# Kernel tuning notes

Measured on AMD Instinct MI355X. Metric: run time of the kernel, lower is better.

Reference implementation:

```python
import jax, jax.numpy as jnp
import numpy as np

EPS = 1e-6
D = 512      # embedding_dim
M = 4        # n_modules
B = 4        # batch
S = 128      # seq_len
K = 32       # stack_size
STEPS = 16   # max_steps (ACT)
SCALE = D ** (-0.5)


def _clin(zr, zi, Wr, Wi, sub):
    # complex linear: (Wr + i Wi)(zr + i zi), torch Linear convention y = x @ W.T
    yr = jnp.einsum(sub, zr, Wr) - jnp.einsum(sub, zi, Wi)
    yi = jnp.einsum(sub, zi, Wr) + jnp.einsum(sub, zr, Wi)
    return yr, yi


def forward_fn(x_real, x_imag, Wl_r, Wl_i, Wq_r, Wq_i, Wk_r, Wk_i, Wv_r, Wv_i,
               ln_scale, ln_shift, mod_bias, gate_mask,
               score_w, score_b, conf_w, conf_b, halt_w, halt_b,
               ctrl_w, ctrl_b, st_score_w, st_score_b, st_conf_w, st_conf_b):
    mem0 = jnp.zeros((B, K, 2 * D), x_real.dtype)
    ptr0 = jnp.zeros((B, K), x_real.dtype).at[:, 0].set(1.0)
    acc0 = jnp.zeros((B, S, 2 * D), x_real.dtype)
    rem0 = jnp.ones((B,), x_real.dtype)

    def step(carry, _):
        sr, si, mem, ptr, acc, rem = carry
        # ComplexAttentionBlock (all M modules vectorized on axis m)
        cr = 0.5 * x_real + 0.5 * sr
        ci = 0.5 * x_imag + 0.5 * si
        zr, zi = _clin(cr, ci, Wl_r, Wl_i, 'bsd,mod->bmso')   # [B,M,S,D]
        # ComplexLayerNorm (magnitude LN, unbiased var as torch.var default)
        mag = jnp.sqrt(zr * zr + zi * zi) + EPS
        mean = mag.mean(-1, keepdims=True)
        var = mag.var(-1, keepdims=True, ddof=1)
        nm = (mag - mean) / jnp.sqrt(var + EPS)
        nm = nm * ln_scale[None, :, None, :] + ln_shift[None, :, None, :]
        ph = jnp.arctan2(zi, zr)
        zr = nm * jnp.cos(ph)
        zi = nm * jnp.sin(ph)
        # ModReLU
        nrm = jnp.sqrt(zr * zr + zi * zi) + EPS
        sc = jax.nn.relu(nrm + mod_bias[None, :, None, :]) / nrm
        zr = zr * sc
        zi = zi * sc
        # ComplexAttention over concatenated real/imag q,k
        sub = 'bmsd,mod->bmso'
        qr, qi = _clin(zr, zi, Wq_r, Wq_i, sub)
        kr, ki = _clin(zr, zi, Wk_r, Wk_i, sub)
        vr, vi = _clin(zr, zi, Wv_r, Wv_i, sub)
        qf = jnp.concatenate([qr, qi], -1)   # [B,M,S,2D]
        kf = jnp.concatenate([kr, ki], -1)
        attn = jax.nn.softmax(jnp.einsum('bmse,bmte->bmst', qf, kf) * SCALE, axis=-1)
        ar = jnp.einsum('bmst,bmtd->bmsd', attn, vr)
        ai = jnp.einsum('bmst,bmtd->bmsd', attn, vi)
        # SigmoidGatingMask
        g = jax.nn.sigmoid(gate_mask)[None, :, None, :]
        pr = ar * g
        pi = ai * g
        flat = jnp.concatenate([pr, pi], -1)  # [B,M,S,2D]
        score = jnp.einsum('bmse,me->bms', flat, score_w) + score_b[None, :, None]
        conf = jax.nn.sigmoid(jnp.einsum('bmse,me->bms', flat, conf_w) + conf_b[None, :, None])
        halt = jnp.einsum('bmse,me->bms', flat, halt_w) + halt_b[None, :, None]
        # DifferentiableStack on seq-pooled broadcast state
        flat_in = jnp.concatenate([sr.mean(1), si.mean(1)], -1)  # [B,2D]
        control = jax.nn.softmax(flat_in @ ctrl_w + ctrl_b, axis=-1)  # [B,3]
        push, pop, noop = control[:, 0:1], control[:, 1:2], control[:, 2:3]
        ptr_up = jnp.roll(ptr, 1, axis=1)
        ptr_dn = jnp.roll(ptr, -1, axis=1)
        new_ptr = push * ptr_up + pop * ptr_dn + noop * ptr
        new_ptr = new_ptr / (new_ptr.sum(1, keepdims=True) + EPS)
        wmask = push * ptr_up                                   # [B,K]
        new_mem = wmask[..., None] * flat_in[:, None, :] + mem * (1.0 - wmask[..., None])
        read = (new_mem * new_ptr[..., None]).sum(1)            # [B,2D]
        sp_r, sp_i = read[:, :D], read[:, D:]
        st_sc = read @ st_score_w + st_score_b[0]               # [B]
        st_cf = jax.nn.sigmoid(read @ st_conf_w + st_conf_b[0])
        # combine M block proposals + stack proposal via score*confidence softmax
        all_pr = jnp.concatenate([pr, jnp.broadcast_to(sp_r[:, None, None, :], (B, 1, S, D))], 1)
        all_pi = jnp.concatenate([pi, jnp.broadcast_to(sp_i[:, None, None, :], (B, 1, S, D))], 1)
        all_sc = jnp.concatenate([score, jnp.broadcast_to(st_sc[:, None, None], (B, 1, S))], 1)
        all_cf = jnp.concatenate([conf, jnp.broadcast_to(st_cf[:, None, None], (B, 1, S))], 1)
        w = jax.nn.softmax(all_sc * all_cf, axis=1)[..., None]  # [B,M+1,S,1]
        new_sr = (w * all_pr).sum(1)
        new_si = (w * all_pi).sum(1)
        # ACT halting accumulation
        p = jax.nn.sigmoid(halt).mean(axis=(1, 2))              # [B]
        acc = acc + (p * rem)[:, None, None] * jnp.concatenate([new_sr, new_si], -1)
        rem = rem * (1.0 - p)
        return (new_sr, new_si, new_mem, new_ptr, acc, rem), None

    carry, _ = jax.lax.scan(step, (x_real, x_imag, mem0, ptr0, acc0, rem0), None, length=STEPS)
    sr, si, _, _, acc, rem = carry
    # add ACT remainder weight on final state
    out = acc + rem[:, None, None] * jnp.concatenate([sr, si], -1)
    return out  # [B,S,2D] real/imag concat


def setup_inputs() -> dict:
    key = jax.random.key(0)
    ks = jax.random.split(key, 24)
    w = 1.0 / np.sqrt(D)
    h = 0.02
    inp = {
        'x_real': jax.random.normal(ks[0], (B, S, D), jnp.float32),
        'x_imag': jax.random.normal(ks[1], (B, S, D), jnp.float32),
        'Wl_r': jax.random.normal(ks[2], (M, D, D), jnp.float32) * w,
        'Wl_i': jax.random.normal(ks[3], (M, D, D), jnp.float32) * w,
        'Wq_r': jax.random.normal(ks[4], (M, D, D), jnp.float32) * w,
        'Wq_i': jax.random.normal(ks[5], (M, D, D), jnp.float32) * w,
        'Wk_r': jax.random.normal(ks[6], (M, D, D), jnp.float32) * w,
        'Wk_i': jax.random.normal(ks[7], (M, D, D), jnp.float32) * w,
        'Wv_r': jax.random.normal(ks[8], (M, D, D), jnp.float32) * w,
        'Wv_i': jax.random.normal(ks[9], (M, D, D), jnp.float32) * w,
        'ln_scale': jnp.ones((M, D), jnp.float32),
        'ln_shift': jnp.zeros((M, D), jnp.float32),
        'mod_bias': jnp.zeros((M, D), jnp.float32),
        'gate_mask': jnp.ones((M, D), jnp.float32),
        'score_w': jax.random.normal(ks[10], (M, 2 * D), jnp.float32) * h,
        'score_b': jnp.zeros((M,), jnp.float32),
        'conf_w': jax.random.normal(ks[11], (M, 2 * D), jnp.float32) * h,
        'conf_b': jnp.zeros((M,), jnp.float32),
        'halt_w': jax.random.normal(ks[12], (M, 2 * D), jnp.float32) * h,
        'halt_b': jnp.full((M,), -4.0, jnp.float32),  # nn.init.constant_(halt_head.bias, -4.0)
        'ctrl_w': jax.random.normal(ks[13], (2 * D, 3), jnp.float32) * h,
        'ctrl_b': jnp.zeros((3,), jnp.float32),
        'st_score_w': jax.random.normal(ks[14], (2 * D,), jnp.float32) * h,
        'st_score_b': jnp.zeros((1,), jnp.float32),
        'st_conf_w': jax.random.normal(ks[15], (2 * D,), jnp.float32) * h,
        'st_conf_b': jnp.zeros((1,), jnp.float32),
    }
    return inp


def reference(x_real, x_imag, Wl_r, Wl_i, Wq_r, Wq_i, Wk_r, Wk_i, Wv_r, Wv_i,
              ln_scale, ln_shift, mod_bias, gate_mask,
              score_w, score_b, conf_w, conf_b, halt_w, halt_b,
              ctrl_w, ctrl_b, st_score_w, st_score_b, st_conf_w, st_conf_b):
    return forward_fn(x_real, x_imag, Wl_r, Wl_i, Wq_r, Wq_i, Wk_r, Wk_i, Wv_r, Wv_i,
                      ln_scale, ln_shift, mod_bias, gate_mask,
                      score_w, score_b, conf_w, conf_b, halt_w, halt_b,
                      ctrl_w, ctrl_b, st_score_w, st_score_b, st_conf_w, st_conf_b)
```

## Files before the change

### kernel.cpp

```cpp
#include <hip/hip_runtime.h>

#define DD 512
#define MM 4
#define BB 4
#define SS 128
#define KK 32
#define NSTEPS 16
#define EPSF 1e-6f
#define SCALEF 0.04419417382415922f

typedef unsigned short u16;
typedef __bf16 bf16x8 __attribute__((ext_vector_type(8)));
typedef u16 u16x8 __attribute__((ext_vector_type(8)));
typedef float f32x16 __attribute__((ext_vector_type(16)));

__device__ inline void split_bf16(float x, u16& h, u16& l) {
  __bf16 hb = (__bf16)x;
  float hf = (float)hb;
  __bf16 lb = (__bf16)(x - hf);
  h = __builtin_bit_cast(u16, hb);
  l = __builtin_bit_cast(u16, lb);
}

__global__ void k_convw(const float* __restrict__ src, u16* __restrict__ dst) {
  int idx = blockIdx.x * 256 + threadIdx.x;
  int row = idx >> 9, k = idx & 511;
  u16 h, l;
  split_bf16(src[idx], h, l);
  dst[(size_t)row * 1024 + k] = h;
  dst[(size_t)row * 1024 + 512 + k] = l;
}

__global__ void k_init(const float* __restrict__ xr, const float* __restrict__ xi,
                       float* __restrict__ sr, float* __restrict__ si,
                       float* __restrict__ acc, float* __restrict__ memv,
                       float* __restrict__ ptrv, float* __restrict__ rem,
                       u16* __restrict__ crbf, u16* __restrict__ cibf) {
  int idx = blockIdx.x * 256 + threadIdx.x;
  if (idx < BB * SS * 2 * DD) acc[idx] = 0.f;
  if (idx < BB * SS * DD) {
    float a = xr[idx], b = xi[idx];
    sr[idx] = a; si[idx] = b;
    int row = idx >> 9, d = idx & 511;
    u16 h, l;
    split_bf16(a, h, l);
    crbf[(size_t)row * 1024 + d] = h;
    crbf[(size_t)row * 1024 + 512 + d] = l;
    split_bf16(b, h, l);
    cibf[(size_t)row * 1024 + d] = h;
    cibf[(size_t)row * 1024 + 512 + d] = l;
  }
  if (idx < BB * KK * 2 * DD) memv[idx] = 0.f;
  if (idx < BB * KK) ptrv[idx] = ((idx & (KK - 1)) == 0) ? 1.f : 0.f;
  if (idx < BB) rem[idx] = 1.f;
}

__global__ void k_flatctrl(const float* __restrict__ sr, const float* __restrict__ si,
                           const float* __restrict__ ctrl_w, const float* __restrict__ ctrl_b,
                           float* __restrict__ ptrv, float* __restrict__ flat_in,
                           float* __restrict__ nptrg, float* __restrict__ wmg,
                           float* __restrict__ stacc) {
  int b = blockIdx.x;
  int tid = threadIdx.x;
  __shared__ float red[3 * 256];
  __shared__ float ctrl[3], optr[KK], nptr_s[KK], wm_s[KK], normf;

  if (tid < KK) optr[tid] = ptrv[b * KK + tid];

  int e4 = tid * 4;
  const float* basep = (e4 < DD) ? sr : si;
  int d4 = (e4 < DD) ? e4 : (e4 - DD);
  float4 accv = make_float4(0.f, 0.f, 0.f, 0.f);
  size_t base = (size_t)b * SS * DD + d4;
  for (int s = 0; s < SS; s++) {
    float4 v = *(const float4*)&basep[base + (size_t)s * DD];
    accv.x += v.x; accv.y += v.y; accv.z += v.z; accv.w += v.w;
  }
  accv.x *= (1.0f / SS); accv.y *= (1.0f / SS); accv.z *= (1.0f / SS); accv.w *= (1.0f / SS);
  *(float4*)&flat_in[b * 2 * DD + e4] = accv;
  float fv[4] = {accv.x, accv.y, accv.z, accv.w};
  float d0 = 0.f, d1 = 0.f, d2 = 0.f;
#pragma unroll
  for (int j = 0; j < 4; j++) {
    d0 += fv[j] * ctrl_w[(e4 + j) * 3 + 0];
    d1 += fv[j] * ctrl_w[(e4 + j) * 3 + 1];
    d2 += fv[j] * ctrl_w[(e4 + j) * 3 + 2];
  }
  red[tid] = d0; red[256 + tid] = d1; red[512 + tid] = d2;
  __syncthreads();
  for (int off = 128; off > 0; off >>= 1) {
    if (tid < off) {
      red[tid] += red[tid + off];
      red[256 + tid] += red[256 + tid + off];
      red[512 + tid] += red[512 + tid + off];
    }
    __syncthreads();
  }
// ... 31 lines not shown
#define LSTR 72

__global__ __launch_bounds__(256) void k_gemm_mfma(
    const u16* __restrict__ Ar, const u16* __restrict__ Ai,
    const u16* __restrict__ Wr, const u16* __restrict__ Wi,
    float* __restrict__ Cr, float* __restrict__ Ci) {
  __shared__ u16 sAr[64][LSTR], sAi[64][LSTR], sWr[64][LSTR], sWi[64][LSTR];
  int m = blockIdx.z;
  int row_blk = blockIdx.y * 64, o_blk = blockIdx.x * 64;
  int tid = threadIdx.x;

  int lrow = tid >> 3, lk8 = (tid & 7) << 3;
  size_t arow0 = (size_t)(row_blk + lrow), arow1 = arow0 + 32;
  size_t wrow0 = (size_t)m * DD + o_blk + lrow, wrow1 = wrow0 + 32;

  int wave = tid >> 6, lane = tid & 63;
  int wrow = (wave >> 1) * 32, wcol = (wave & 1) * 32;
  int l31 = lane & 31, khalf = (lane >> 5) * 8;

  f32x16 accP, accN, accI;
  for (int i = 0; i < 16; i++) { accP[i] = 0.f; accN[i] = 0.f; accI[i] = 0.f; }

  u16x8 g0 = *(const u16x8*)&Ar[arow0 * 1024 + lk8];
  u16x8 g1 = *(const u16x8*)&Ar[arow1 * 1024 + lk8];
  u16x8 g2 = *(const u16x8*)&Ai[arow0 * 1024 + lk8];
  u16x8 g3 = *(const u16x8*)&Ai[arow1 * 1024 + lk8];
  u16x8 g4 = *(const u16x8*)&Wr[wrow0 * 1024 + lk8];
  u16x8 g5 = *(const u16x8*)&Wr[wrow1 * 1024 + lk8];
  u16x8 g6 = *(const u16x8*)&Wi[wrow0 * 1024 + lk8];
  u16x8 g7 = *(const u16x8*)&Wi[wrow1 * 1024 + lk8];

  for (int it = 0; it < 24; ++it) {
    __syncthreads();
    *(u16x8*)&sAr[lrow][lk8] = g0;
    *(u16x8*)&sAr[lrow + 32][lk8] = g1;
    *(u16x8*)&sAi[lrow][lk8] = g2;
    *(u16x8*)&sAi[lrow + 32][lk8] = g3;
    *(u16x8*)&sWr[lrow][lk8] = g4;
    *(u16x8*)&sWr[lrow + 32][lk8] = g5;
    *(u16x8*)&sWi[lrow][lk8] = g6;
    *(u16x8*)&sWi[lrow + 32][lk8] = g7;
    u16x8 n0, n1, n2, n3, n4, n5, n6, n7;
    if (it < 23) {
      int it2 = it + 1, seg = it2 >> 3, k0 = (it2 & 7) * 64;
      int aofs = (seg == 1) ? 512 : 0, wofs = (seg == 2) ? 512 : 0;
      n0 = *(const u16x8*)&Ar[arow0 * 1024 + aofs + k0 + lk8];
      n1 = *(const u16x8*)&Ar[arow1 * 1024 + aofs + k0 + lk8];
      n2 = *(const u16x8*)&Ai[arow0 * 1024 + aofs + k0 + lk8];
      n3 = *(const u16x8*)&Ai[arow1 * 1024 + aofs + k0 + lk8];
      n4 = *(const u16x8*)&Wr[wrow0 * 1024 + wofs + k0 + lk8];
      n5 = *(const u16x8*)&Wr[wrow1 * 1024 + wofs + k0 + lk8];
      n6 = *(const u16x8*)&Wi[wrow0 * 1024 + wofs + k0 + lk8];
      n7 = *(const u16x8*)&Wi[wrow1 * 1024 + wofs + k0 + lk8];
    }
    __syncthreads();
#pragma unroll
    for (int kk = 0; kk < 64; kk += 16) {
      bf16x8 fAr = *(const bf16x8*)&sAr[wrow + l31][kk + khalf];
      bf16x8 fAi = *(const bf16x8*)&sAi[wrow + l31][kk + khalf];
      bf16x8 fWr = *(const bf16x8*)&sWr[wcol + l31][kk + khalf];
      bf16x8 fWi = *(const bf16x8*)&sWi[wcol + l31][kk + khalf];
      accP = __builtin_amdgcn_mfma_f32_32x32x16_bf16(fAr, fWr, accP, 0, 0, 0);
      accN = __builtin_amdgcn_mfma_f32_32x32x16_bf16(fAi, fWi, accN, 0, 0, 0);
      accI = __builtin_amdgcn_mfma_f32_32x32x16_bf16(fAi, fWr, accI, 0, 0, 0);
      accI = __builtin_amdgcn_mfma_f32_32x32x16_bf16(fAr, fWi, accI, 0, 0, 0);
    }
    if (it < 23) {
      g0 = n0; g1 = n1; g2 = n2; g3 = n3; g4 = n4; g5 = n5; g6 = n6; g7 = n7;
    }
  }

  int o = o_blk + wcol + l31;
#pragma unroll
  for (int reg = 0; reg < 16; reg++) {
    int r_in = (reg & 3) + 8 * (reg >> 2) + 4 * (lane >> 5);
    int gr = row_blk + wrow + r_in;
    int b = gr >> 7, s = gr & (SS - 1);
    size_t crow = (size_t)((b * MM + m) * SS + s);
    Cr[crow * DD + o] = accP[reg] - accN[reg];
    Ci[crow * DD + o] = accI[reg];
  }
}

__global__ __launch_bounds__(256) void k_gemm_qkv(
    const u16* __restrict__ Ar, const u16* __restrict__ Ai,
    const u16* __restrict__ wbf, size_t WSLOT,
    u16* __restrict__ qbr, u16* __restrict__ qbi,
    u16* __restrict__ kbr, u16* __restrict__ kbi,
    u16* __restrict__ vbr, u16* __restrict__ vbi) {
  __shared__ u16 sAr[64][LSTR], sAi[64][LSTR], sWr[64][LSTR], sWi[64][LSTR];
  int zid = blockIdx.z;
  int m = zid / 3, w = zid - 3 * m;
  const u16* Wr = wbf + (size_t)(2 + 2 * w) * WSLOT;
  const u16* Wi = Wr + WSLOT;
  int row_blk = blockIdx.y * 64, o_blk = blockIdx.x * 64;
  int tid = threadIdx.x;

  int lrow = tid >> 3, lk8 = (tid & 7) << 3;
  int gr0 = row_blk + lrow, gr1 = gr0 + 32;
  size_t arow0 = (size_t)(((gr0 >> 7) * MM + m) * SS + (gr0 & (SS - 1)));
  size_t arow1 = (size_t)(((gr1 >> 7) * MM + m) * SS + (gr1 & (SS - 1)));
  size_t wrow0 = (size_t)m * DD + o_blk + lrow, wrow1 = wrow0 + 32;

  int wave = tid >> 6, lane = tid & 63;
  int wrow = (wave >> 1) * 32, wcol = (wave & 1) * 32;
  int l31 = lane & 31, khalf = (lane >> 5) * 8;

  f32x16 accP, accN, accI;
  for (int i = 0; i < 16; i++) { accP[i] = 0.f; accN[i] = 0.f; accI[i] = 0.f; }

  u16x8 g0 = *(const u16x8*)&Ar[arow0 * 1024 + lk8];
  u16x8 g1 = *(const u16x8*)&Ar[arow1 * 1024 + lk8];
  u16x8 g2 = *(const u16x8*)&Ai[arow0 * 1024 + lk8];
  u16x8 g3 = *(const u16x8*)&Ai[arow1 * 1024 + lk8];
  u16x8 g4 = *(const u16x8*)&Wr[wrow0 * 1024 + lk8];
  u16x8 g5 = *(const u16x8*)&Wr[wrow1 * 1024 + lk8];
  u16x8 g6 = *(const u16x8*)&Wi[wrow0 * 1024 + lk8];
  u16x8 g7 = *(const u16x8*)&Wi[wrow1 * 1024 + lk8];

  for (int it = 0; it < 24; ++it) {
    __syncthreads();
    *(u16x8*)&sAr[lrow][lk8] = g0;
    *(u16x8*)&sAr[lrow + 32][lk8] = g1;
    *(u16x8*)&sAi[lrow][lk8] = g2;
    *(u16x8*)&sAi[lrow + 32][lk8] = g3;
    *(u16x8*)&sWr[lrow][lk8] = g4;
    *(u16x8*)&sWr[lrow + 32][lk8] = g5;
    *(u16x8*)&sWi[lrow][lk8] = g6;
    *(u16x8*)&sWi[lrow + 32][lk8] = g7;
    u16x8 n0, n1, n2, n3, n4, n5, n6, n7;
    if (it < 23) {
      int it2 = it + 1, seg = it2 >> 3, k0 = (it2 & 7) * 64;
      int aofs = (seg == 1) ? 512 : 0, wofs = (seg == 2) ? 512 : 0;
      n0 = *(const u16x8*)&Ar[arow0 * 1024 + aofs + k0 + lk8];
      n1 = *(const u16x8*)&Ar[arow1 * 1024 + aofs + k0 + lk8];
      n2 = *(const u16x8*)&Ai[arow0 * 1024 + aofs + k0 + lk8];
      n3 = *(const u16x8*)&Ai[arow1 * 1024 + aofs + k0 + lk8];
      n4 = *(const u16x8*)&Wr[wrow0 * 1024 + wofs + k0 + lk8];
      n5 = *(const u16x8*)&Wr[wrow1 * 1024 + wofs + k0 + lk8];
      n6 = *(const u16x8*)&Wi[wrow0 * 1024 + wofs + k0 + lk8];
      n7 = *(const u16x8*)&Wi[wrow1 * 1024 + wofs + k0 + lk8];
    }
    __syncthreads();
#pragma unroll
    for (int kk = 0; kk < 64; kk += 16) {
      bf16x8 fAr = *(const bf16x8*)&sAr[wrow + l31][kk + khalf];
      bf16x8 fAi = *(const bf16x8*)&sAi[wrow + l31][kk + khalf];
      bf16x8 fWr = *(const bf16x8*)&sWr[wcol + l31][kk + khalf];
      bf16x8 fWi = *(const bf16x8*)&sWi[wcol + l31][kk + khalf];
      accP = __builtin_amdgcn_mfma_f32_32x32x16_bf16(fAr, fWr, accP, 0, 0, 0);
      accN = __builtin_amdgcn_mfma_f32_32x32x16_bf16(fAi, fWi, accN, 0, 0, 0);
      accI = __builtin_amdgcn_mfma_f32_32x32x16_bf16(fAi, fWr, accI, 0, 0, 0);
      accI = __builtin_amdgcn_mfma_f32_32x32x16_bf16(fAr, fWi, accI, 0, 0, 0);
    }
    if (it < 23) {
      g0 = n0; g1 = n1; g2 = n2; g3 = n3; g4 = n4; g5 = n5; g6 = n6; g7 = n7;
    }
  }

  u16* Cr = (w == 0) ? qbr : ((w == 1) ? kbr : vbr);
  u16* Ci = (w == 0) ? qbi : ((w == 1) ? kbi : vbi);
  int o = o_blk + wcol + l31;
#pragma unroll
  for (int reg = 0; reg < 16; reg++) {
    int r_in = (reg & 3) + 8 * (reg >> 2) + 4 * (lane >> 5);
    int gr = row_blk + wrow + r_in;
    int b = gr >> 7, s = gr & (SS - 1);
    size_t crow = (size_t)((b * MM + m) * SS + s);
    u16 h, l;
    split_bf16(accP[reg] - accN[reg], h, l);
    Cr[crow * 1024 + o] = h;
    Cr[crow * 1024 + 512 + o] = l;
    split_bf16(accI[reg], h, l);
    Ci[crow * 1024 + o] = h;
    Ci[crow * 1024 + 512 + o] = l;
  }
}

__global__ __launch_bounds__(256) void k_scores_sm(
    const u16* __restrict__ Q_r, const u16* __restrict__ Q_i,
    const u16* __restrict__ K_r, const u16* __restrict__ K_i,
    u16* __restrict__ Pb) {
  __shared__ __align__(16) char smem[55296];
  u16 (*sQr)[LSTR] = (u16(*)[LSTR])smem;
  u16 (*sQi)[LSTR] = (u16(*)[LSTR])(smem + 9216);
  u16 (*sKr)[LSTR] = (u16(*)[LSTR])(smem + 18432);
  u16 (*sKi)[LSTR] = (u16(*)[LSTR])(smem + 36864);
  float (*stile)[132] = (float(*)[132])smem;

  int bm = blockIdx.z;
  int s_blk = blockIdx.y * 64;
  int tid = threadIdx.x;
  int lrow = tid >> 3, lk8 = (tid & 7) << 3;
  size_t qrow0 = (size_t)(bm * SS + s_blk + lrow), qrow1 = qrow0 + 32;
  size_t krow = (size_t)(bm * SS + lrow);

  int wave = tid >> 6, lane = tid & 63;
  int srow_w = (wave & 1) * 32;
  int tcol_w = (wave >> 1) * 64;
  int l31 = lane & 31, khalf = (lane >> 5) * 8;

  f32x16 acc0, acc1;
  for (int i = 0; i < 16; i++) { acc0[i] = 0.f; acc1[i] = 0.f; }

  for (int it = 0; it < 24; ++it) {
    int seg = it >> 3, k0 = (it & 7) * 64;
    int qofs = (seg == 1) ? 512 : 0;
    int kofs = (seg == 2) ? 512 : 0;
    u16x8 q0 = *(const u16x8*)&Q_r[qrow0 * 1024 + qofs + k0 + lk8];
    u16x8 q1 = *(const u16x8*)&Q_r[qrow1 * 1024 + qofs + k0 + lk8];
    u16x8 q2 = *(const u16x8*)&Q_i[qrow0 * 1024 + qofs + k0 + lk8];
    u16x8 q3 = *(const u16x8*)&Q_i[qrow1 * 1024 + qofs + k0 + lk8];
    u16x8 kr0 = *(const u16x8*)&K_r[(krow + 0) * 1024 + kofs + k0 + lk8];
    u16x8 kr1 = *(const u16x8*)&K_r[(krow + 32) * 1024 + kofs + k0 + lk8];
    u16x8 kr2 = *(const u16x8*)&K_r[(krow + 64) * 1024 + kofs + k0 + lk8];
    u16x8 kr3 = *(const u16x8*)&K_r[(krow + 96) * 1024 + kofs + k0 + lk8];
    u16x8 ki0 = *(const u16x8*)&K_i[(krow + 0) * 1024 + kofs + k0 + lk8];
    u16x8 ki1 = *(const u16x8*)&K_i[(krow + 32) * 1024 + kofs + k0 + lk8];
    u16x8 ki2 = *(const u16x8*)&K_i[(krow + 64) * 1024 + kofs + k0 + lk8];
    u16x8 ki3 = *(const u16x8*)&K_i[(krow + 96) * 1024 + kofs + k0 + lk8];
    __syncthreads();
    *(u16x8*)&sQr[lrow][lk8] = q0;
    *(u16x8*)&sQr[lrow + 32][lk8] = q1;
    *(u16x8*)&sQi[lrow][lk8] = q2;
    *(u16x8*)&sQi[lrow + 32][lk8] = q3;
    *(u16x8*)&sKr[lrow][lk8] = kr0;
    *(u16x8*)&sKr[lrow + 32][lk8] = kr1;
    *(u16x8*)&sKr[lrow + 64][lk8] = kr2;
    *(u16x8*)&sKr[lrow + 96][lk8] = kr3;
    *(u16x8*)&sKi[lrow][lk8] = ki0;
    *(u16x8*)&sKi[lrow + 32][lk8] = ki1;
    *(u16x8*)&sKi[lrow + 64][lk8] = ki2;
    *(u16x8*)&sKi[lrow + 96][lk8] = ki3;
    __syncthreads();
#pragma unroll
    for (int kk = 0; kk < 64; kk += 16) {
      bf16x8 fQr = *(const bf16x8*)&sQr[srow_w + l31][kk + khalf];
      bf16x8 fQi = *(const bf16x8*)&sQi[srow_w + l31][kk + khalf];
      bf16x8 fKr0 = *(const bf16x8*)&sKr[tcol_w + l31][kk + khalf];
      bf16x8 fKr1 = *(const bf16x8*)&sKr[tcol_w + 32 + l31][kk + khalf];
      bf16x8 fKi0 = *(const bf16x8*)&sKi[tcol_w + l31][kk + khalf];
      bf16x8 fKi1 = *(const bf16x8*)&sKi[tcol_w + 32 + l31][kk + khalf];
      acc0 = __builtin_amdgcn_mfma_f32_32x32x16_bf16(fQr, fKr0, acc0, 0, 0, 0);
      acc0 = __builtin_amdgcn_mfma_f32_32x32x16_bf16(fQi, fKi0, acc0, 0, 0, 0);
      acc1 = __builtin_amdgcn_mfma_f32_32x32x16_bf16(fQr, fKr1, acc1, 0, 0, 0);
      acc1 = __builtin_amdgcn_mfma_f32_32x32x16_bf16(fQi, fKi1, acc1, 0, 0, 0);
    }
  }

  __syncthreads();
#pragma unroll
  for (int reg = 0; reg < 16; reg++) {
    int r = srow_w + (reg & 3) + 8 * (reg >> 2) + 4 * (lane >> 5);
    stile[r][tcol_w + l31] = acc0[reg] * SCALEF;
    stile[r][tcol_w + 32 + l31] = acc1[reg] * SCALEF;
  }
  __syncthreads();
  int row = tid >> 2;
// ... 300 lines not shown
}

extern "C" void kernel_launch(void* const* d_in, const int* in_sizes, int n_in,
                              void* d_out, int out_size, void* d_ws, size_t ws_size,
                              hipStream_t stream) {
  const float* xr = (const float*)d_in[0];
  const float* xi = (const float*)d_in[1];
  const float* Wl_r = (const float*)d_in[2];
  const float* Wl_i = (const float*)d_in[3];
  const float* Wq_r = (const float*)d_in[4];
  const float* Wq_i = (const float*)d_in[5];
  const float* Wk_r = (const float*)d_in[6];
  const float* Wk_i = (const float*)d_in[7];
  const float* Wv_r = (const float*)d_in[8];
  const float* Wv_i = (const float*)d_in[9];
  const float* ln_scale = (const float*)d_in[10];
  const float* ln_shift = (const float*)d_in[11];
  const float* mod_bias = (const float*)d_in[12];
  const float* gate_mask = (const float*)d_in[13];
  const float* score_w = (const float*)d_in[14];
  const float* score_b = (const float*)d_in[15];
  const float* conf_w = (const float*)d_in[16];
  const float* conf_b = (const float*)d_in[17];
  const float* halt_w = (const float*)d_in[18];
  const float* halt_b = (const float*)d_in[19];
  const float* ctrl_w = (const float*)d_in[20];
  const float* ctrl_b = (const float*)d_in[21];
  const float* st_score_w = (const float*)d_in[22];
  const float* st_score_b = (const float*)d_in[23];
  const float* st_conf_w = (const float*)d_in[24];
  const float* st_conf_b = (const float*)d_in[25];
  float* out = (float*)d_out;

  const int BSD = BB * SS * DD;
  const int BMSD = BB * MM * SS * DD;
  const size_t WSLOT = (size_t)MM * DD * 1024;

  char* pc = (char*)d_ws;
  float* sr = (float*)pc; pc += (size_t)BSD * 4;
  float* si = (float*)pc; pc += (size_t)BSD * 4;
  float* zr = (float*)pc; pc += (size_t)BMSD * 4;
  float* zi = (float*)pc; pc += (size_t)BMSD * 4;
  float* prb = (float*)pc; pc += (size_t)BMSD * 4;
  float* pib = (float*)pc; pc += (size_t)BMSD * 4;
  float* scorev = (float*)pc; pc += (size_t)BB * MM * SS * 4;
  float* confv = (float*)pc; pc += (size_t)BB * MM * SS * 4;
  float* haltv = (float*)pc; pc += (size_t)BB * MM * SS * 4;
  float* flat = (float*)pc; pc += (size_t)BB * 2 * DD * 4;
  float* stacc = (float*)pc; pc += 64;
  float* nptrg = (float*)pc; pc += (size_t)BB * KK * 4;
  float* wmg = (float*)pc; pc += (size_t)BB * KK * 4;
  float* memv = (float*)pc; pc += (size_t)BB * KK * 2 * DD * 4;
  float* ptrv = (float*)pc; pc += (size_t)BB * KK * 4;
  float* readv = (float*)pc; pc += (size_t)BB * 2 * DD * 4;
  float* stv = (float*)pc; pc += (size_t)2 * BB * 4;
  float* accb = (float*)pc; pc += (size_t)BB * SS * 2 * DD * 4;
  float* rem = (float*)pc; pc += (size_t)BB * 4;
  float* coeff = (float*)pc; pc += (size_t)BB * 4;
  u16* crbf = (u16*)pc; pc += (size_t)BB * SS * 1024 * 2;
  u16* cibf = (u16*)pc; pc += (size_t)BB * SS * 1024 * 2;
  u16* zbr = (u16*)pc; pc += (size_t)BB * MM * SS * 1024 * 2;
  u16* zbi = (u16*)pc; pc += (size_t)BB * MM * SS * 1024 * 2;
  u16* qbr = (u16*)pc; pc += (size_t)BB * MM * SS * 1024 * 2;
  u16* qbi = (u16*)pc; pc += (size_t)BB * MM * SS * 1024 * 2;
  u16* kbr = (u16*)pc; pc += (size_t)BB * MM * SS * 1024 * 2;
  u16* kbi = (u16*)pc; pc += (size_t)BB * MM * SS * 1024 * 2;
  u16* vbr = (u16*)pc; pc += (size_t)BB * MM * SS * 1024 * 2;
  u16* vbi = (u16*)pc; pc += (size_t)BB * MM * SS * 1024 * 2;
  u16* Pb  = (u16*)pc; pc += (size_t)BB * MM * SS * 256 * 2;
  u16* wbf = (u16*)pc; pc += 8 * WSLOT * 2;

  k_convw<<<4096, 256, 0, stream>>>(Wl_r, wbf + 0 * WSLOT);
  k_convw<<<4096, 256, 0, stream>>>(Wl_i, wbf + 1 * WSLOT);
  k_convw<<<4096, 256, 0, stream>>>(Wq_r, wbf + 2 * WSLOT);
  k_convw<<<4096, 256, 0, stream>>>(Wq_i, wbf + 3 * WSLOT);
  k_convw<<<4096, 256, 0, stream>>>(Wk_r, wbf + 4 * WSLOT);
  k_convw<<<4096, 256, 0, stream>>>(Wk_i, wbf + 5 * WSLOT);
  k_convw<<<4096, 256, 0, stream>>>(Wv_r, wbf + 6 * WSLOT);
  k_convw<<<4096, 256, 0, stream>>>(Wv_i, wbf + 7 * WSLOT);

  k_init<<<2048, 256, 0, stream>>>(xr, xi, sr, si, accb, memv, ptrv, rem, crbf, cibf);

  dim3 ggrid(DD / 64, (BB * SS) / 64, MM);
  dim3 qgrid(DD / 64, (BB * SS) / 64, MM * 3);
  dim3 smgrid(1, SS / 64, BB * MM);
  dim3 pvgrid(DD / 64, SS / 64, BB * MM);

  for (int step = 0; step < NSTEPS; ++step) {
    k_flatctrl<<<BB, 256, 0, stream>>>(sr, si, ctrl_w, ctrl_b, ptrv, flat, nptrg, wmg, stacc);
    k_gemm_mfma<<<ggrid, 256, 0, stream>>>(crbf, cibf, wbf + 0 * WSLOT, wbf + 1 * WSLOT, zr, zi);
    k_lnphase<<<BB * MM * SS, 128, 0, stream>>>(zr, zi, ln_scale, ln_shift, mod_bias, zbr, zbi);
    k_gemm_qkv<<<qgrid, 256, 0, stream>>>(zbr, zbi, wbf, WSLOT, qbr, qbi, kbr, kbi, vbr, vbi);
    k_scores_sm<<<smgrid, 256, 0, stream>>>(qbr, qbi, kbr, kbi, Pb);
    k_pv<<<pvgrid, 256, 0, stream>>>(Pb, vbr, vbi, gate_mask, prb, pib);
    k_heads<<<BB * MM * SS, 256, 0, stream>>>(prb, pib, score_w, score_b, conf_w, conf_b,
                                              halt_w, halt_b, scorev, confv, haltv);
    k_memup<<<BB * 4, 256, 0, stream>>>(flat, nptrg, wmg, memv, readv,
                                        st_score_w, st_conf_w, stacc);
    k_haltp<<<BB, 256, 0, stream>>>(haltv, rem, coeff, stacc, st_score_b, st_conf_b, stv);
    k_combine<<<BB * SS, 256, 0, stream>>>(prb, pib, scorev, confv, stv, readv, coeff,
                                           xr, xi, sr, si, accb, crbf, cibf);
  }

  k_final<<<(BB * SS * 2 * DD) / 256, 256, 0, stream>>>(accb, rem, sr, si, out);
}
```

Baseline: 2.512 ms.

## Enlarge QKV GEMM tiles to 128x128 with XOR-swizzled LDS and sign-flipped MFMA

The complex QKV GEMM moves from 64x64 to 128x128 block tiles, with each wave computing a 2x2 set of 32x32 MFMA sub-tiles. This raises data reuse per LDS load and cuts global traffic. Shared memory drops the padded stride in favour of an XOR swizzle to avoid bank conflicts. The real-part subtraction is folded into the accumulator by flipping the bf16 sign bits of Ai, so one accumulator replaces two. The cost is far fewer blocks (192 instead of 768), which lowers occupancy and parallelism, plus higher register pressure from eight accumulators and 16 prefetch vectors.

```diff
diff --git a/kernel.cpp b/kernel.cpp
--- a/kernel.cpp
+++ b/kernel.cpp
@@ -13,6 +13,7 @@
 typedef __bf16 bf16x8 __attribute__((ext_vector_type(8)));
 typedef u16 u16x8 __attribute__((ext_vector_type(8)));
 typedef float f32x16 __attribute__((ext_vector_type(16)));
+typedef unsigned int u32x4 __attribute__((ext_vector_type(4)));
 
 __device__ inline void split_bf16(float x, u16& h, u16& l) {
   __bf16 hb = (__bf16)x;
@@ -210,98 +211,137 @@
   }
 }
 
-__global__ __launch_bounds__(256) void k_gemm_qkv(
+__global__ __launch_bounds__(256, 1) void k_gemm_qkv(
     const u16* __restrict__ Ar, const u16* __restrict__ Ai,
     const u16* __restrict__ wbf, size_t WSLOT,
     u16* __restrict__ qbr, u16* __restrict__ qbi,
     u16* __restrict__ kbr, u16* __restrict__ kbi,
     u16* __restrict__ vbr, u16* __restrict__ vbi) {
-  __shared__ u16 sAr[64][LSTR], sAi[64][LSTR], sWr[64][LSTR], sWi[64][LSTR];
+  __shared__ u16 smem[4][128][64];
+  u16* sm = &smem[0][0][0];
   int zid = blockIdx.z;
   int m = zid / 3, w = zid - 3 * m;
   const u16* Wr = wbf + (size_t)(2 + 2 * w) * WSLOT;
   const u16* Wi = Wr + WSLOT;
-  int row_blk = blockIdx.y * 64, o_blk = blockIdx.x * 64;
-  int tid = threadIdx.x;
-
-  int lrow = tid >> 3, lk8 = (tid & 7) << 3;
-  int gr0 = row_blk + lrow, gr1 = gr0 + 32;
-  size_t arow0 = (size_t)(((gr0 >> 7) * MM + m) * SS + (gr0 & (SS - 1)));
-  size_t arow1 = (size_t)(((gr1 >> 7) * MM + m) * SS + (gr1 & (SS - 1)));
-  size_t wrow0 = (size_t)m * DD + o_blk + lrow, wrow1 = wrow0 + 32;
-
+  int b = blockIdx.y;
+  int o_blk = blockIdx.x * 128;
+  int tid = threadIdx.x;
+
+  size_t abase = (size_t)(b * MM + m) * SS;
+  size_t wbase = (size_t)m * DD + o_blk;
+
+  int row = tid >> 3;
+  int e8 = tid & 7;
   int wave = tid >> 6, lane = tid & 63;
-  int wrow = (wave >> 1) * 32, wcol = (wave & 1) * 32;
-  int l31 = lane & 31, khalf = (lane >> 5) * 8;
-
-  f32x16 accP, accN, accI;
-  for (int i = 0; i < 16; i++) { accP[i] = 0.f; accN[i] = 0.f; accI[i] = 0.f; }
-
-  u16x8 g0 = *(const u16x8*)&Ar[arow0 * 1024 + lk8];
-  u16x8 g1 = *(const u16x8*)&Ar[arow1 * 1024 + lk8];
-  u16x8 g2 = *(const u16x8*)&Ai[arow0 * 1024 + lk8];
-  u16x8 g3 = *(const u16x8*)&Ai[arow1 * 1024 + lk8];
-  u16x8 g4 = *(const u16x8*)&Wr[wrow0 * 1024 + lk8];
-  u16x8 g5 = *(const u16x8*)&Wr[wrow1 * 1024 + lk8];
-  u16x8 g6 = *(const u16x8*)&Wi[wrow0 * 1024 + lk8];
-  u16x8 g7 = *(const u16x8*)&Wi[wrow1 * 1024 + lk8];
+  int wr = wave >> 1, wc = wave & 1;
+  int l31 = lane & 31, hi = lane >> 5;
+  int x7 = l31 & 7;
+
+  int rA0 = (wr * 64 + l31) * 64;
+  int rA1 = rA0 + 32 * 64;
+  int rW0 = (wc * 64 + l31) * 64;
+  int rW1 = rW0 + 32 * 64;
+
+  f32x16 aR00, aR01, aR10, aR11, aI00, aI01, aI10, aI11;
+  for (int i = 0; i < 16; i++) {
+    aR00[i] = 0.f; aR01[i] = 0.f; aR10[i] = 0.f; aR11[i] = 0.f;
+    aI00[i] = 0.f; aI01[i] = 0.f; aI10[i] = 0.f; aI11[i] = 0.f;
+  }
+
+  u16x8 pf[16];
+#pragma unroll
+  for (int q = 0; q < 4; q++) {
+    int r = row + q * 32;
+    int sb = (e8 ^ (r & 7)) * 8;
+    pf[0 * 4 + q] = *(const u16x8*)&Ar[(abase + r) * 1024 + sb];
+    pf[1 * 4 + q] = *(const u16x8*)&Ai[(abase + r) * 1024 + sb];
+    pf[2 * 4 + q] = *(const u16x8*)&Wr[(wbase + r) * 1024 + sb];
+    pf[3 * 4 + q] = *(const u16x8*)&Wi[(wbase + r) * 1024 + sb];
+  }
 
   for (int it = 0; it < 24; ++it) {
     __syncthreads();
-    *(u16x8*)&sAr[lrow][lk8] = g0;
-    *(u16x8*)&sAr[lrow + 32][lk8] = g1;
-    *(u16x8*)&sAi[lrow][lk8] = g2;
-    *(u16x8*)&sAi[lrow + 32][lk8] = g3;
-    *(u16x8*)&sWr[lrow][lk8] = g4;
-    *(u16x8*)&sWr[lrow + 32][lk8] = g5;
-    *(u16x8*)&sWi[lrow][lk8] = g6;
-    *(u16x8*)&sWi[lrow + 32][lk8] = g7;
-    u16x8 n0, n1, n2, n3, n4, n5, n6, n7;
+#pragma unroll
+    for (int p = 0; p < 4; p++) {
+#pragma unroll
+      for (int q = 0; q < 4; q++) {
+        int idx = q * 32 + row;
+        *(u16x8*)&sm[p * 8192 + idx * 64 + e8 * 8] = pf[p * 4 + q];
+      }
+    }
+    u16x8 nf[16];
     if (it < 23) {
       int it2 = it + 1, seg = it2 >> 3, k0 = (it2 & 7) * 64;
       int aofs = (seg == 1) ? 512 : 0, wofs = (seg == 2) ? 512 : 0;
-      n0 = *(const u16x8*)&Ar[arow0 * 1024 + aofs + k0 + lk8];
-      n1 = *(const u16x8*)&Ar[arow1 * 1024 + aofs + k0 + lk8];
-      n2 = *(const u16x8*)&Ai[arow0 * 1024 + aofs + k0 + lk8];
-      n3 = *(const u16x8*)&Ai[arow1 * 1024 + aofs + k0 + lk8];
-      n4 = *(const u16x8*)&Wr[wrow0 * 1024 + wofs + k0 + lk8];
-      n5 = *(const u16x8*)&Wr[wrow1 * 1024 + wofs + k0 + lk8];
-      n6 = *(const u16x8*)&Wi[wrow0 * 1024 + wofs + k0 + lk8];
-      n7 = *(const u16x8*)&Wi[wrow1 * 1024 + wofs + k0 + lk8];
-    }
-    __syncthreads();
-#pragma unroll
-    for (int kk = 0; kk < 64; kk += 16) {
-      bf16x8 fAr = *(const bf16x8*)&sAr[wrow + l31][kk + khalf];
-      bf16x8 fAi = *(const bf16x8*)&sAi[wrow + l31][kk + khalf];
-      bf16x8 fWr = *(const bf16x8*)&sWr[wcol + l31][kk + khalf];
-      bf16x8 fWi = *(const bf16x8*)&sWi[wcol + l31][kk + khalf];
-      accP = __builtin_amdgcn_mfma_f32_32x32x16_bf16(fAr, fWr, accP, 0, 0, 0);
-      accN = __builtin_amdgcn_mfma_f32_32x32x16_bf16(fAi, fWi, accN, 0, 0, 0);
-      accI = __builtin_amdgcn_mfma_f32_32x32x16_bf16(fAi, fWr, accI, 0, 0, 0);
-      accI = __builtin_amdgcn_mfma_f32_32x32x16_bf16(fAr, fWi, accI, 0, 0, 0);
+#pragma unroll
+      for (int q = 0; q < 4; q++) {
+        int r = row + q * 32;
+        int sb = (e8 ^ (r & 7)) * 8;
+        nf[0 * 4 + q] = *(const u16x8*)&Ar[(abase + r) * 1024 + aofs + k0 + sb];
+        nf[1 * 4 + q] = *(const u16x8*)&Ai[(abase + r) * 1024 + aofs + k0 + sb];
+        nf[2 * 4 + q] = *(const u16x8*)&Wr[(wbase + r) * 1024 + wofs + k0 + sb];
+        nf[3 * 4 + q] = *(const u16x8*)&Wi[(wbase + r) * 1024 + wofs + k0 + sb];
+      }
+    }
+    __syncthreads();
+#pragma unroll
+    for (int kk = 0; kk < 4; kk++) {
+      int koff = ((kk * 2 + hi) ^ x7) * 8;
+      bf16x8 fAr0 = *(const bf16x8*)&sm[0 * 8192 + rA0 + koff];
+      bf16x8 fAr1 = *(const bf16x8*)&sm[0 * 8192 + rA1 + koff];
+      bf16x8 fAi0 = *(const bf16x8*)&sm[1 * 8192 + rA0 + koff];
+      bf16x8 fAi1 = *(const bf16x8*)&sm[1 * 8192 + rA1 + koff];
+      bf16x8 fWr0 = *(const bf16x8*)&sm[2 * 8192 + rW0 + koff];
+      bf16x8 fWr1 = *(const bf16x8*)&sm[2 * 8192 + rW1 + koff];
+      bf16x8 fWi0 = *(const bf16x8*)&sm[3 * 8192 + rW0 + koff];
+      bf16x8 fWi1 = *(const bf16x8*)&sm[3 * 8192 + rW1 + koff];
+      u32x4 t0 = __builtin_bit_cast(u32x4, fAi0) ^ 0x80008000u;
+      u32x4 t1 = __builtin_bit_cast(u32x4, fAi1) ^ 0x80008000u;
+      bf16x8 nAi0 = __builtin_bit_cast(bf16x8, t0);
+      bf16x8 nAi1 = __builtin_bit_cast(bf16x8, t1);
+      aR00 = __builtin_amdgcn_mfma_f32_32x32x16_bf16(fAr0, fWr0, aR00, 0, 0, 0);
+      aR00 = __builtin_amdgcn_mfma_f32_32x32x16_bf16(nAi0, fWi0, aR00, 0, 0, 0);
+      aI00 = __builtin_amdgcn_mfma_f32_32x32x16_bf16(fAi0, fWr0, aI00, 0, 0, 0);
+      aI00 = __builtin_amdgcn_mfma_f32_32x32x16_bf16(fAr0, fWi0, aI00, 0, 0, 0);
+      aR01 = __builtin_amdgcn_mfma_f32_32x32x16_bf16(fAr0, fWr1, aR01, 0, 0, 0);
+      aR01 = __builtin_amdgcn_mfma_f32_32x32x16_bf16(nAi0, fWi1, aR01, 0, 0, 0);
+      aI01 = __builtin_amdgcn_mfma_f32_32x32x16_bf16(fAi0, fWr1, aI01, 0, 0, 0);
+      aI01 = __builtin_amdgcn_mfma_f32_32x32x16_bf16(fAr0, fWi1, aI01, 0, 0, 0);
+      aR10 = __builtin_amdgcn_mfma_f32_32x32x16_bf16(fAr1, fWr0, aR10, 0, 0, 0);
+      aR10 = __builtin_amdgcn_mfma_f32_32x32x16_bf16(nAi1, fWi0, aR10, 0, 0, 0);
+      aI10 = __builtin_amdgcn_mfma_f32_32x32x16_bf16(fAi1, fWr0, aI10, 0, 0, 0);
+      aI10 = __builtin_amdgcn_mfma_f32_32x32x16_bf16(fAr1, fWi0, aI10, 0, 0, 0);
+      aR11 = __builtin_amdgcn_mfma_f32_32x32x16_bf16(fAr1, fWr1, aR11, 0, 0, 0);
+      aR11 = __builtin_amdgcn_mfma_f32_32x32x16_bf16(nAi1, fWi1, aR11, 0, 0, 0);
+      aI11 = __builtin_amdgcn_mfma_f32_32x32x16_bf16(fAi1, fWr1, aI11, 0, 0, 0);
+      aI11 = __builtin_amdgcn_mfma_f32_32x32x16_bf16(fAr1, fWi1, aI11, 0, 0, 0);
     }
     if (it < 23) {
-      g0 = n0; g1 = n1; g2 = n2; g3 = n3; g4 = n4; g5 = n5; g6 = n6; g7 = n7;
+#pragma unroll
+      for (int j = 0; j < 16; j++) pf[j] = nf[j];
     }
   }
 
   u16* Cr = (w == 0) ? qbr : ((w == 1) ? kbr : vbr);
   u16* Ci = (w == 0) ? qbi : ((w == 1) ? kbi : vbi);
-  int o = o_blk + wcol + l31;
+  int o0 = o_blk + wc * 64 + l31;
+  int o1 = o0 + 32;
 #pragma unroll
   for (int reg = 0; reg < 16; reg++) {
-    int r_in = (reg & 3) + 8 * (reg >> 2) + 4 * (lane >> 5);
-    int gr = row_blk + wrow + r_in;
-    int b = gr >> 7, s = gr & (SS - 1);
-    size_t crow = (size_t)((b * MM + m) * SS + s);
+    int r_in = (reg & 3) + 8 * (reg >> 2) + 4 * hi;
+    int s0 = wr * 64 + r_in;
+    int s1 = s0 + 32;
+    size_t row0 = (abase + s0) * 1024;
+    size_t row1 = (abase + s1) * 1024;
     u16 h, l;
-    split_bf16(accP[reg] - accN[reg], h, l);
-    Cr[crow * 1024 + o] = h;
-    Cr[crow * 1024 + 512 + o] = l;
-    split_bf16(accI[reg], h, l);
-    Ci[crow * 1024 + o] = h;
-    Ci[crow * 1024 + 512 + o] = l;
+    split_bf16(aR00[reg], h, l); Cr[row0 + o0] = h; Cr[row0 + 512 + o0] = l;
+    split_bf16(aI00[reg], h, l); Ci[row0 + o0] = h; Ci[row0 + 512 + o0] = l;
+    split_bf16(aR01[reg], h, l); Cr[row0 + o1] = h; Cr[row0 + 512 + o1] = l;
+    split_bf16(aI01[reg], h, l); Ci[row0 + o1] = h; Ci[row0 + 512 + o1] = l;
+    split_bf16(aR10[reg], h, l); Cr[row1 + o0] = h; Cr[row1 + 512 + o0] = l;
+    split_bf16(aI10[reg], h, l); Ci[row1 + o0] = h; Ci[row1 + 512 + o0] = l;
+    split_bf16(aR11[reg], h, l); Cr[row1 + o1] = h; Cr[row1 + 512 + o1] = l;
+    split_bf16(aI11[reg], h, l); Ci[row1 + o1] = h; Ci[row1 + 512 + o1] = l;
   }
 }
 
@@ -768,7 +808,7 @@
   k_init<<<2048, 256, 0, stream>>>(xr, xi, sr, si, accb, memv, ptrv, rem, crbf, cibf);
 
   dim3 ggrid(DD / 64, (BB * SS) / 64, MM);
-  dim3 qgrid(DD / 64, (BB * SS) / 64, MM * 3);
+  dim3 qgrid(DD / 128, (BB * SS) / 128, MM * 3);
   dim3 smgrid(1, SS / 64, BB * MM);
   dim3 pvgrid(DD / 64, SS / 64, BB * MM);
 
```

New measurement: 2.548 ms. No clear change (+1.4%).

## Widen QKV GEMM tile to 128 output columns and fold sign into operand

Applied to the files above, without the earlier changes.

The complex QKV projection GEMM now gives each block 128 output columns instead of 64, so each wave computes two 32x32 output subtiles. Each A-fragment load from shared memory is therefore reused across twice as many MFMAs. The real-part subtraction is moved into the MFMA by flipping the sign bits of the imaginary A fragment, which removes one accumulator per subtile. The cost is more shared memory and registers per block and half as many blocks (384), which may lower occupancy and the number of CUs kept busy.

```diff
diff --git a/kernel.cpp b/kernel.cpp
--- a/kernel.cpp
+++ b/kernel.cpp
@@ -13,6 +13,7 @@
 typedef __bf16 bf16x8 __attribute__((ext_vector_type(8)));
 typedef u16 u16x8 __attribute__((ext_vector_type(8)));
 typedef float f32x16 __attribute__((ext_vector_type(16)));
+typedef unsigned int u32x4 __attribute__((ext_vector_type(4)));
 
 __device__ inline void split_bf16(float x, u16& h, u16& l) {
   __bf16 hb = (__bf16)x;
@@ -216,92 +217,103 @@
     u16* __restrict__ qbr, u16* __restrict__ qbi,
     u16* __restrict__ kbr, u16* __restrict__ kbi,
     u16* __restrict__ vbr, u16* __restrict__ vbi) {
-  __shared__ u16 sAr[64][LSTR], sAi[64][LSTR], sWr[64][LSTR], sWi[64][LSTR];
+  __shared__ u16 sAr[64][LSTR], sAi[64][LSTR], sWr[128][LSTR], sWi[128][LSTR];
   int zid = blockIdx.z;
   int m = zid / 3, w = zid - 3 * m;
   const u16* Wr = wbf + (size_t)(2 + 2 * w) * WSLOT;
   const u16* Wi = Wr + WSLOT;
-  int row_blk = blockIdx.y * 64, o_blk = blockIdx.x * 64;
+  int row_blk = blockIdx.y * 64, o_blk = blockIdx.x * 128;
   int tid = threadIdx.x;
 
   int lrow = tid >> 3, lk8 = (tid & 7) << 3;
   int gr0 = row_blk + lrow, gr1 = gr0 + 32;
   size_t arow0 = (size_t)(((gr0 >> 7) * MM + m) * SS + (gr0 & (SS - 1)));
   size_t arow1 = (size_t)(((gr1 >> 7) * MM + m) * SS + (gr1 & (SS - 1)));
-  size_t wrow0 = (size_t)m * DD + o_blk + lrow, wrow1 = wrow0 + 32;
+  size_t wrowb = (size_t)m * DD + o_blk + lrow;
 
   int wave = tid >> 6, lane = tid & 63;
-  int wrow = (wave >> 1) * 32, wcol = (wave & 1) * 32;
+  int wrow = (wave >> 1) * 32, wcol = (wave & 1) * 64;
   int l31 = lane & 31, khalf = (lane >> 5) * 8;
 
-  f32x16 accP, accN, accI;
-  for (int i = 0; i < 16; i++) { accP[i] = 0.f; accN[i] = 0.f; accI[i] = 0.f; }
-
-  u16x8 g0 = *(const u16x8*)&Ar[arow0 * 1024 + lk8];
-  u16x8 g1 = *(const u16x8*)&Ar[arow1 * 1024 + lk8];
-  u16x8 g2 = *(const u16x8*)&Ai[arow0 * 1024 + lk8];
-  u16x8 g3 = *(const u16x8*)&Ai[arow1 * 1024 + lk8];
-  u16x8 g4 = *(const u16x8*)&Wr[wrow0 * 1024 + lk8];
-  u16x8 g5 = *(const u16x8*)&Wr[wrow1 * 1024 + lk8];
-  u16x8 g6 = *(const u16x8*)&Wi[wrow0 * 1024 + lk8];
-  u16x8 g7 = *(const u16x8*)&Wi[wrow1 * 1024 + lk8];
+  f32x16 aR0, aI0, aR1, aI1;
+  for (int i = 0; i < 16; i++) { aR0[i] = 0.f; aI0[i] = 0.f; aR1[i] = 0.f; aI1[i] = 0.f; }
+
+  u16x8 pf[12];
+  pf[0] = *(const u16x8*)&Ar[arow0 * 1024 + lk8];
+  pf[1] = *(const u16x8*)&Ar[arow1 * 1024 + lk8];
+  pf[2] = *(const u16x8*)&Ai[arow0 * 1024 + lk8];
+  pf[3] = *(const u16x8*)&Ai[arow1 * 1024 + lk8];
+#pragma unroll
+  for (int q = 0; q < 4; q++) {
+    pf[4 + q] = *(const u16x8*)&Wr[(wrowb + q * 32) * 1024 + lk8];
+    pf[8 + q] = *(const u16x8*)&Wi[(wrowb + q * 32) * 1024 + lk8];
+  }
 
   for (int it = 0; it < 24; ++it) {
     __syncthreads();
-    *(u16x8*)&sAr[lrow][lk8] = g0;
-    *(u16x8*)&sAr[lrow + 32][lk8] = g1;
-    *(u16x8*)&sAi[lrow][lk8] = g2;
-    *(u16x8*)&sAi[lrow + 32][lk8] = g3;
-    *(u16x8*)&sWr[lrow][lk8] = g4;
-    *(u16x8*)&sWr[lrow + 32][lk8] = g5;
-    *(u16x8*)&sWi[lrow][lk8] = g6;
-    *(u16x8*)&sWi[lrow + 32][lk8] = g7;
-    u16x8 n0, n1, n2, n3, n4, n5, n6, n7;
+    *(u16x8*)&sAr[lrow][lk8] = pf[0];
+    *(u16x8*)&sAr[lrow + 32][lk8] = pf[1];
+    *(u16x8*)&sAi[lrow][lk8] = pf[2];
+    *(u16x8*)&sAi[lrow + 32][lk8] = pf[3];
+#pragma unroll
+    for (int q = 0; q < 4; q++) {
+      *(u16x8*)&sWr[lrow + q * 32][lk8] = pf[4 + q];
+      *(u16x8*)&sWi[lrow + q * 32][lk8] = pf[8 + q];
+    }
+    u16x8 nf[12];
     if (it < 23) {
       int it2 = it + 1, seg = it2 >> 3, k0 = (it2 & 7) * 64;
       int aofs = (seg == 1) ? 512 : 0, wofs = (seg == 2) ? 512 : 0;
-      n0 = *(const u16x8*)&Ar[arow0 * 1024 + aofs + k0 + lk8];
-      n1 = *(const u16x8*)&Ar[arow1 * 1024 + aofs + k0 + lk8];
-      n2 = *(const u16x8*)&Ai[arow0 * 1024 + aofs + k0 + lk8];
-      n3 = *(const u16x8*)&Ai[arow1 * 1024 + aofs + k0 + lk8];
-      n4 = *(const u16x8*)&Wr[wrow0 * 1024 + wofs + k0 + lk8];
-      n5 = *(const u16x8*)&Wr[wrow1 * 1024 + wofs + k0 + lk8];
-      n6 = *(const u16x8*)&Wi[wrow0 * 1024 + wofs + k0 + lk8];
-      n7 = *(const u16x8*)&Wi[wrow1 * 1024 + wofs + k0 + lk8];
+      nf[0] = *(const u16x8*)&Ar[arow0 * 1024 + aofs + k0 + lk8];
+      nf[1] = *(const u16x8*)&Ar[arow1 * 1024 + aofs + k0 + lk8];
+      nf[2] = *(const u16x8*)&Ai[arow0 * 1024 + aofs + k0 + lk8];
+      nf[3] = *(const u16x8*)&Ai[arow1 * 1024 + aofs + k0 + lk8];
+#pragma unroll
+      for (int q = 0; q < 4; q++) {
+        nf[4 + q] = *(const u16x8*)&Wr[(wrowb + q * 32) * 1024 + wofs + k0 + lk8];
+        nf[8 + q] = *(const u16x8*)&Wi[(wrowb + q * 32) * 1024 + wofs + k0 + lk8];
+      }
     }
     __syncthreads();
 #pragma unroll
     for (int kk = 0; kk < 64; kk += 16) {
       bf16x8 fAr = *(const bf16x8*)&sAr[wrow + l31][kk + khalf];
       bf16x8 fAi = *(const bf16x8*)&sAi[wrow + l31][kk + khalf];
-      bf16x8 fWr = *(const bf16x8*)&sWr[wcol + l31][kk + khalf];
-      bf16x8 fWi = *(const bf16x8*)&sWi[wcol + l31][kk + khalf];
-      accP = __builtin_amdgcn_mfma_f32_32x32x16_bf16(fAr, fWr, accP, 0, 0, 0);
-      accN = __builtin_amdgcn_mfma_f32_32x32x16_bf16(fAi, fWi, accN, 0, 0, 0);
-      accI = __builtin_amdgcn_mfma_f32_32x32x16_bf16(fAi, fWr, accI, 0, 0, 0);
-      accI = __builtin_amdgcn_mfma_f32_32x32x16_bf16(fAr, fWi, accI, 0, 0, 0);
+      bf16x8 fWr0 = *(const bf16x8*)&sWr[wcol + l31][kk + khalf];
+      bf16x8 fWr1 = *(const bf16x8*)&sWr[wcol + 32 + l31][kk + khalf];
+      bf16x8 fWi0 = *(const bf16x8*)&sWi[wcol + l31][kk + khalf];
+      bf16x8 fWi1 = *(const bf16x8*)&sWi[wcol + 32 + l31][kk + khalf];
+      u32x4 t = __builtin_bit_cast(u32x4, fAi) ^ 0x80008000u;
+      bf16x8 nAi = __builtin_bit_cast(bf16x8, t);
+      aR0 = __builtin_amdgcn_mfma_f32_32x32x16_bf16(fAr, fWr0, aR0, 0, 0, 0);
+      aR0 = __builtin_amdgcn_mfma_f32_32x32x16_bf16(nAi, fWi0, aR0, 0, 0, 0);
+      aI0 = __builtin_amdgcn_mfma_f32_32x32x16_bf16(fAi, fWr0, aI0, 0, 0, 0);
+      aI0 = __builtin_amdgcn_mfma_f32_32x32x16_bf16(fAr, fWi0, aI0, 0, 0, 0);
+      aR1 = __builtin_amdgcn_mfma_f32_32x32x16_bf16(fAr, fWr1, aR1, 0, 0, 0);
+      aR1 = __builtin_amdgcn_mfma_f32_32x32x16_bf16(nAi, fWi1, aR1, 0, 0, 0);
+      aI1 = __builtin_amdgcn_mfma_f32_32x32x16_bf16(fAi, fWr1, aI1, 0, 0, 0);
+      aI1 = __builtin_amdgcn_mfma_f32_32x32x16_bf16(fAr, fWi1, aI1, 0, 0, 0);
     }
     if (it < 23) {
-      g0 = n0; g1 = n1; g2 = n2; g3 = n3; g4 = n4; g5 = n5; g6 = n6; g7 = n7;
+#pragma unroll
+      for (int j = 0; j < 12; j++) pf[j] = nf[j];
     }
   }
 
   u16* Cr = (w == 0) ? qbr : ((w == 1) ? kbr : vbr);
   u16* Ci = (w == 0) ? qbi : ((w == 1) ? kbi : vbi);
-  int o = o_blk + wcol + l31;
+  int o0 = o_blk + wcol + l31;
 #pragma unroll
   for (int reg = 0; reg < 16; reg++) {
     int r_in = (reg & 3) + 8 * (reg >> 2) + 4 * (lane >> 5);
     int gr = row_blk + wrow + r_in;
     int b = gr >> 7, s = gr & (SS - 1);
-    size_t crow = (size_t)((b * MM + m) * SS + s);
+    size_t crow = (size_t)((b * MM + m) * SS + s) * 1024;
     u16 h, l;
-    split_bf16(accP[reg] - accN[reg], h, l);
-    Cr[crow * 1024 + o] = h;
-    Cr[crow * 1024 + 512 + o] = l;
-    split_bf16(accI[reg], h, l);
-    Ci[crow * 1024 + o] = h;
-    Ci[crow * 1024 + 512 + o] = l;
+    split_bf16(aR0[reg], h, l); Cr[crow + o0] = h; Cr[crow + 512 + o0] = l;
+    split_bf16(aI0[reg], h, l); Ci[crow + o0] = h; Ci[crow + 512 + o0] = l;
+    split_bf16(aR1[reg], h, l); Cr[crow + o0 + 32] = h; Cr[crow + 512 + o0 + 32] = l;
+    split_bf16(aI1[reg], h, l); Ci[crow + o0 + 32] = h; Ci[crow + 512 + o0 + 32] = l;
   }
 }
 
@@ -768,7 +780,7 @@
   k_init<<<2048, 256, 0, stream>>>(xr, xi, sr, si, accb, memv, ptrv, rem, crbf, cibf);
 
   dim3 ggrid(DD / 64, (BB * SS) / 64, MM);
-  dim3 qgrid(DD / 64, (BB * SS) / 64, MM * 3);
+  dim3 qgrid(DD / 128, (BB * SS) / 64, MM * 3);
   dim3 smgrid(1, SS / 64, BB * MM);
   dim3 pvgrid(DD / 64, SS / 64, BB * MM);
 
```

New measurement: 2.463 ms. About the same (-2.0%).
